# Kernel tuning notes

Hardware: AMD Instinct MI355X
Metric: run time of the kernel (lower is better)

## Reference

```python
import jax, jax.numpy as jnp
import numpy as np

THRESHOLD = 0.3          # config.sparse_threshold
COMPETITION_FACTOR = 2.0 # config.competition_factor
TARGET_SPARSITY = 0.1    # config.target_sparsity


def setup_inputs() -> dict:
    key = jax.random.key(0)
    B, D = 32768, 1024
    H = D // 4
    ks = jax.random.split(key, 18)
    def lin(k, fan_in, shape):
        return jax.random.normal(k, shape, dtype=jnp.float32) / np.sqrt(fan_in)
    return {
        "features": jax.random.normal(ks[0], (B, D), dtype=jnp.float32),
        # sparse_gating: Linear(D, D//4) -> ReLU -> Linear(D//4, D) -> Sigmoid
        "w_g1": lin(ks[1], D, (D, H)), "b_g1": jnp.zeros((H,), jnp.float32),
        "w_g2": lin(ks[2], H, (H, D)), "b_g2": jnp.zeros((D,), jnp.float32),
        # competition_calculator: Linear(D, D) -> ReLU -> Linear(D, 1) -> Sigmoid
        "w_c1": lin(ks[3], D, (D, D)), "b_c1": jnp.zeros((D,), jnp.float32),
        "w_c2": lin(ks[4], D, (D, 1)), "b_c2": jnp.zeros((1,), jnp.float32),
        # sparsity_feedback: Linear(2, 16) -> ReLU -> Linear(16, D) -> Sigmoid
        "w_r1": lin(ks[5], 2, (2, 16)), "b_r1": jnp.zeros((16,), jnp.float32),
        "w_r2": lin(ks[6], 16, (16, D)), "b_r2": jnp.zeros((D,), jnp.float32),
        # adaptive_threshold: Linear(3, 16) -> ReLU -> Linear(16, 1) -> Sigmoid
        "w_m1": lin(ks[7], 3, (3, 16)), "b_m1": jnp.zeros((16,), jnp.float32),
        "w_m2": lin(ks[8], 16, (16, 1)), "b_m2": jnp.zeros((1,), jnp.float32),
    }


def _competitive_sparse(f, w_c1, b_c1, w_c2, b_c2):
    # competition_strength: [B, 1] scalar per row (output Linear has out_dim 1)
    c = jax.nn.sigmoid(jax.nn.relu(f @ w_c1 + b_c1) @ w_c2 + b_c2)  # [B,1]
    inh = COMPETITION_FACTOR * c                                     # [B,1]
    # other_activations_j = f_j * (1 - inh) for j != i, and f_i at position i.
    scaled = f * (1.0 - inh)                                         # [B,D]
    # max over j != i of scaled_j, vectorized via top-2
    top2_vals, _ = jax.lax.top_k(scaled, 2)                          # [B,2]
    am = jnp.argmax(scaled, axis=-1)                                 # [B]
    idx = jnp.arange(f.shape[-1])
    max_excl = jnp.where(idx[None, :] == am[:, None],
                         top2_vals[:, 1:2], top2_vals[:, 0:1])       # [B,D]
    other_max = jnp.maximum(f, max_excl)                             # includes own f_i term
    win = other_max < f
    return jnp.where(f > THRESHOLD, jnp.where(win, f, 0.0), f)


def reference(features, w_g1, b_g1, w_g2, b_g2, w_c1, b_c1, w_c2, b_c2,
              w_r1, b_r1, w_r2, b_r2, w_m1, b_m1, w_m2, b_m2):
    # 1) sparse gating
    gw = jax.nn.sigmoid(jax.nn.relu(features @ w_g1 + b_g1) @ w_g2 + b_g2)
    gated = features * gw
    # 2) competitive sparse activation
    comp = _competitive_sparse(gated, w_c1, b_c1, w_c2, b_c2)
    # 3) dynamic sparsity regulation
    cur_sp = jnp.mean((jnp.abs(comp) < 0.1).astype(comp.dtype), axis=-1)  # [B]
    sp_in = jnp.stack([cur_sp, jnp.full_like(cur_sp, TARGET_SPARSITY)], axis=-1)  # [B,2]
    rw = jax.nn.sigmoid(jax.nn.relu(sp_in @ w_r1 + b_r1) @ w_r2 + b_r2)  # [B,D]
    dyn = comp * rw
    # 4) adaptive threshold (monitor); torch.std is unbiased -> ddof=1
    fmean = jnp.mean(dyn, axis=-1, keepdims=True)
    fstd = jnp.std(dyn, axis=-1, ddof=1, keepdims=True)
    fmax = jnp.max(dyn, axis=-1, keepdims=True)
    thr_in = jnp.concatenate([fmean, fstd, fmax], axis=-1)            # [B,3]
    thr = jax.nn.sigmoid(jax.nn.relu(thr_in @ w_m1 + b_m1) @ w_m2 + b_m2)  # [B,1]
    # 5) final sparse mask
    mask = (jnp.abs(dyn) > thr).astype(dyn.dtype)
    return dyn * mask
```

## Files before the change

### kernel.cpp

```cpp
#include <hip/hip_runtime.h>
#include <cmath>

#define TM 128
#define TN 128
#define TK 16
#define LDSW 132
#define BAND 1e-4
#define FIXCAP 262144u

#define STAGE_STORE(B)                                                          \
        As[B][aq * 4 + 0][ar] = pa0.x; As[B][aq * 4 + 1][ar] = pa0.y;           \
        As[B][aq * 4 + 2][ar] = pa0.z; As[B][aq * 4 + 3][ar] = pa0.w;           \
        As[B][aq * 4 + 0][ar + 64] = pa1.x; As[B][aq * 4 + 1][ar + 64] = pa1.y; \
        As[B][aq * 4 + 2][ar + 64] = pa1.z; As[B][aq * 4 + 3][ar + 64] = pa1.w; \
        *(float4*)&Bs[B][bk][bn4] = pb0;                                        \
        *(float4*)&Bs[B][bk + 8][bn4] = pb1;

#define GEMM_MAINLOOP(Aptr, Wptr, Kdim, Ndim)                                   \
    __shared__ float As[2][TK][LDSW];                                           \
    __shared__ float Bs[2][TK][LDSW];                                           \
    const int tid = threadIdx.x;                                                \
    const int bm = blockIdx.x * TM;                                             \
    const int bn = blockIdx.y * TN;                                             \
    const int tx = tid & 15, ty = tid >> 4;                                     \
    const int ar = tid >> 2, aq = tid & 3;                                      \
    const int bk = tid >> 5, bn4 = (tid & 31) * 4;                              \
    float acc[2][2][4][4];                                                      \
    _Pragma("unroll") for (int a = 0; a < 2; ++a)                               \
    _Pragma("unroll") for (int b = 0; b < 2; ++b)                               \
    _Pragma("unroll") for (int i = 0; i < 4; ++i)                               \
    _Pragma("unroll") for (int j = 0; j < 4; ++j) acc[a][b][i][j] = 0.f;        \
    float4 pa0 = *(const float4*)((Aptr) + (size_t)(bm + ar) * (Kdim) + aq * 4);      \
    float4 pa1 = *(const float4*)((Aptr) + (size_t)(bm + ar + 64) * (Kdim) + aq * 4); \
    float4 pb0 = *(const float4*)((Wptr) + (size_t)bk * (Ndim) + bn + bn4);           \
    float4 pb1 = *(const float4*)((Wptr) + (size_t)(bk + 8) * (Ndim) + bn + bn4);     \
    STAGE_STORE(0)                                                              \
    __syncthreads();                                                            \
    int buf = 0;                                                                \
    for (int k0 = 0; k0 < (Kdim); k0 += TK) {                                   \
        const int nk = k0 + TK;                                                 \
        if (nk < (Kdim)) {                                                      \
            pa0 = *(const float4*)((Aptr) + (size_t)(bm + ar) * (Kdim) + nk + aq * 4);      \
            pa1 = *(const float4*)((Aptr) + (size_t)(bm + ar + 64) * (Kdim) + nk + aq * 4); \
            pb0 = *(const float4*)((Wptr) + (size_t)(nk + bk) * (Ndim) + bn + bn4);         \
            pb1 = *(const float4*)((Wptr) + (size_t)(nk + bk + 8) * (Ndim) + bn + bn4);     \
        }                                                                       \
        _Pragma("unroll") for (int k = 0; k < TK; ++k) {                        \
            float4 da0 = *(const float4*)&As[buf][k][ty * 4];                   \
            float4 da1 = *(const float4*)&As[buf][k][64 + ty * 4];              \
            float4 db0 = *(const float4*)&Bs[buf][k][tx * 4];                   \
            float4 db1 = *(const float4*)&Bs[buf][k][64 + tx * 4];              \
            const float* dap[2] = {&da0.x, &da1.x};                             \
            const float* dbp[2] = {&db0.x, &db1.x};                             \
            _Pragma("unroll") for (int a = 0; a < 2; ++a)                       \
            _Pragma("unroll") for (int b = 0; b < 2; ++b)                       \
            _Pragma("unroll") for (int i = 0; i < 4; ++i)                       \
            _Pragma("unroll") for (int j = 0; j < 4; ++j)                       \
                acc[a][b][i][j] = fmaf(dap[a][i], dbp[b][j], acc[a][b][i][j]);  \
        }                                                                       \
        if (nk < (Kdim)) {                                                      \
            const int nb = buf ^ 1;                                             \
            STAGE_STORE(nb)                                                     \
            __syncthreads();                                                    \
            buf = nb;                                                           \
        }                                                                       \
    }

__global__ __launch_bounds__(256) void gemm1_f32(
    const float* __restrict__ A, const float* __restrict__ W,
    const float* __restrict__ bias, float* __restrict__ out, int M)
{
    const int K = 1024, N = 256;
    GEMM_MAINLOOP(A, W, K, N)
    #pragma unroll
    for (int a = 0; a < 2; ++a) {
        #pragma unroll
        for (int b = 0; b < 2; ++b) {
            const int col = bn + b * 64 + tx * 4;
            float4 bi = *(const float4*)(bias + col);
            #pragma unroll
            for (int i = 0; i < 4; ++i) {
                const int row = bm + a * 64 + ty * 4 + i;
                float4 o;
                o.x = fmaxf(acc[a][b][i][0] + bi.x, 0.f);
                o.y = fmaxf(acc[a][b][i][1] + bi.y, 0.f);
                o.z = fmaxf(acc[a][b][i][2] + bi.z, 0.f);
                o.w = fmaxf(acc[a][b][i][3] + bi.w, 0.f);
                *(float4*)(out + (size_t)row * N + col) = o;
            }
        }
    }
}

__global__ __launch_bounds__(256) void gemm2_f32(
    const float* __restrict__ A, const float* __restrict__ W,
    const float* __restrict__ bias, const float* __restrict__ F,
    float* __restrict__ out, unsigned* __restrict__ counter,
    uint2* __restrict__ list, int M)
{
    const int K = 256, N = 1024;
    GEMM_MAINLOOP(A, W, K, N)
    #pragma unroll
    for (int a = 0; a < 2; ++a) {
        #pragma unroll
        for (int b = 0; b < 2; ++b) {
            const int col = bn + b * 64 + tx * 4;
            float4 bi = *(const float4*)(bias + col);
            const float* bip = &bi.x;
            #pragma unroll
            for (int i = 0; i < 4; ++i) {
                const int row = bm + a * 64 + ty * 4 + i;
                float4 fv = *(const float4*)(F + (size_t)row * N + col);
                const float* fvp = &fv.x;
                float4 o;
                float* op = &o.x;
                #pragma unroll
                for (int j = 0; j < 4; ++j) {
                    double z = (double)acc[a][b][i][j] + (double)bip[j];
                    double gw = 1.0 / (1.0 + exp(-z));
                    double g = (double)fvp[j] * gw;
                    if (fabs(g - 0.3) < BAND) {
                        unsigned idx = atomicAdd(counter, 1u);
                        if (idx < FIXCAP) list[idx] = make_uint2((unsigned)row, (unsigned)(col + j));
                    }
                    double c = (g > 0.3) ? 0.0 : g;
                    op[j] = (float)c;
                }
                *(float4*)(out + (size_t)row * N + col) = o;
            }
        }
    }
}

__global__ __launch_bounds__(256) void fix_exact(
    const float* __restrict__ F, const float* __restrict__ Wg1,
    const float* __restrict__ bg1, const float* __restrict__ Wg2,
    const float* __restrict__ bg2, const unsigned* __restrict__ counter,
    const uint2* __restrict__ list, float* __restrict__ out)
{
    __shared__ float Fs[1024];
    __shared__ double red[4];
    const int tid = threadIdx.x;
    unsigned cnt = *counter;
    if (cnt > FIXCAP) cnt = FIXCAP;

    for (unsigned e = blockIdx.x; e < cnt; e += gridDim.x) {
        const unsigned row = list[e].x, col = list[e].y;
        *(float4*)&Fs[tid * 4] = *(const float4*)(F + (size_t)row * 1024 + tid * 4);
        __syncthreads();
        double acc = 0.0;
        #pragma unroll 4
        for (int j = 0; j < 1024; ++j)
            acc += (double)Fs[j] * (double)Wg1[(size_t)j * 256 + tid];
        double h = acc + (double)bg1[tid];
        h = (h > 0.0) ? h : 0.0;
        double p = h * (double)Wg2[(size_t)tid * 1024 + col];
        #pragma unroll
        for (int o = 32; o > 0; o >>= 1) p += __shfl_down(p, o, 64);
        if ((tid & 63) == 0) red[tid >> 6] = p;
        __syncthreads();
        if (tid == 0) {
            double z2 = red[0] + red[1] + red[2] + red[3] + (double)bg2[col];
            double gw = 1.0 / (1.0 + exp(-z2));
            double g = (double)Fs[col] * gw;
            double c = (g > 0.3) ? 0.0 : g;
            out[(size_t)row * 1024 + col] = (float)c;
        }
        __syncthreads();
    }
}

__global__ __launch_bounds__(256) void finalize_rows(
    float* __restrict__ C,
    const float* __restrict__ wr1, const float* __restrict__ br1,
    const float* __restrict__ wr2, const float* __restrict__ br2,
    const float* __restrict__ wm1, const float* __restrict__ bm1,
    const float* __restrict__ wm2, const float* __restrict__ bm2)
{
    const int D = 1024;
    const int tid = threadIdx.x;
    const int lane = tid & 63;
    const size_t row = (size_t)blockIdx.x * 4 + (tid >> 6);
    const size_t base = row * D;
    const int col0 = lane * 4;

    float4 c4[4];
    #pragma unroll
    for (int q = 0; q < 4; ++q)
        c4[q] = *(const float4*)(C + base + q * 256 + col0);

    double c[16];
    #pragma unroll
    for (int q = 0; q < 4; ++q) {
        c[q * 4 + 0] = (double)c4[q].x; c[q * 4 + 1] = (double)c4[q].y;
        c[q * 4 + 2] = (double)c4[q].z; c[q * 4 + 3] = (double)c4[q].w;
    }

    double cnt = 0.0;
    #pragma unroll
    for (int i = 0; i < 16; ++i) cnt += (fabs(c[i]) < 0.1) ? 1.0 : 0.0;
    #pragma unroll
    for (int o = 32; o > 0; o >>= 1) cnt += __shfl_xor(cnt, o, 64);
    double cur_sp = cnt / 1024.0;

    double hid[16];
    #pragma unroll
    for (int h = 0; h < 16; ++h) {
        double z = cur_sp * (double)wr1[h] + 0.1 * (double)wr1[16 + h] + (double)br1[h];
        hid[h] = (z > 0.0) ? z : 0.0;
    }

    double dyn[16];
    #pragma unroll
    for (int q = 0; q < 4; ++q) {
        const int cq = q * 256 + col0;
        float4 b4 = *(const float4*)(br2 + cq);
        double z[4] = {(double)b4.x, (double)b4.y, (double)b4.z, (double)b4.w};
        #pragma unroll
        for (int h = 0; h < 16; ++h) {
            float4 w4 = *(const float4*)(wr2 + (size_t)h * D + cq);
            z[0] += hid[h] * (double)w4.x;
            z[1] += hid[h] * (double)w4.y;
            z[2] += hid[h] * (double)w4.z;
            z[3] += hid[h] * (double)w4.w;
        }
        #pragma unroll
        for (int j = 0; j < 4; ++j) {
            double rw = 1.0 / (1.0 + exp(-z[j]));
            dyn[q * 4 + j] = c[q * 4 + j] * rw;
        }
    }

    double s = 0.0, mx = -1e300;
    #pragma unroll
    for (int i = 0; i < 16; ++i) { s += dyn[i]; mx = fmax(mx, dyn[i]); }
    #pragma unroll
    for (int o = 32; o > 0; o >>= 1) s += __shfl_xor(s, o, 64);
    double mean = s / 1024.0;

    double sq = 0.0;
    #pragma unroll
    for (int i = 0; i < 16; ++i) { double d = dyn[i] - mean; sq += d * d; }
    #pragma unroll
    for (int o = 32; o > 0; o >>= 1) sq += __shfl_xor(sq, o, 64);
    double sd = sqrt(sq / 1023.0);

    #pragma unroll
    for (int o = 32; o > 0; o >>= 1) mx = fmax(mx, __shfl_xor(mx, o, 64));

    double acc2 = (double)bm2[0];
    #pragma unroll
    for (int h = 0; h < 16; ++h) {
        double hz = mean * (double)wm1[h] + sd * (double)wm1[16 + h]
                  + mx * (double)wm1[32 + h] + (double)bm1[h];
        hz = (hz > 0.0) ? hz : 0.0;
        acc2 += hz * (double)wm2[h];
    }
    double thr = 1.0 / (1.0 + exp(-acc2));

    #pragma unroll
    for (int q = 0; q < 4; ++q) {
        float4 o4;
        o4.x = (float)((fabs(dyn[q * 4 + 0]) > thr) ? dyn[q * 4 + 0] : 0.0);
        o4.y = (float)((fabs(dyn[q * 4 + 1]) > thr) ? dyn[q * 4 + 1] : 0.0);
        o4.z = (float)((fabs(dyn[q * 4 + 2]) > thr) ? dyn[q * 4 + 2] : 0.0);
        o4.w = (float)((fabs(dyn[q * 4 + 3]) > thr) ? dyn[q * 4 + 3] : 0.0);
        *(float4*)(C + base + q * 256 + col0) = o4;
    }
}

extern "C" void kernel_launch(void* const* d_in, const int* in_sizes, int n_in,
                              void* d_out, int out_size, void* d_ws, size_t ws_size,
                              hipStream_t stream)
{
    const float* F   = (const float*)d_in[0];
    const float* wg1 = (const float*)d_in[1];
    const float* bg1 = (const float*)d_in[2];
    const float* wg2 = (const float*)d_in[3];
    const float* bg2 = (const float*)d_in[4];
    const float* wr1 = (const float*)d_in[9];
    const float* br1 = (const float*)d_in[10];
    const float* wr2 = (const float*)d_in[11];
    const float* br2 = (const float*)d_in[12];
    const float* wm1 = (const float*)d_in[13];
    const float* bm1 = (const float*)d_in[14];
    const float* wm2 = (const float*)d_in[15];
    const float* bm2 = (const float*)d_in[16];

    float* out = (float*)d_out;
    const int M = in_sizes[0] / 1024;

    float*    h1      = (float*)d_ws;
    uint2*    list    = (uint2*)((char*)d_ws + (32u << 20));
    unsigned* counter = (unsigned*)((char*)d_ws + (34u << 20));

    hipMemsetAsync(counter, 0, sizeof(unsigned), stream);
    gemm1_f32<<<dim3(M / TM, 256 / TN), 256, 0, stream>>>(F, wg1, bg1, h1, M);
    gemm2_f32<<<dim3(M / TM, 1024 / TN), 256, 0, stream>>>(h1, wg2, bg2, F, out, counter, list, M);
    fix_exact<<<2048, 256, 0, stream>>>(F, wg1, bg1, wg2, bg2, counter, list, out);
    finalize_rows<<<M / 4, 256, 0, stream>>>(out, wr1, br1, wr2, br2, wm1, bm1, wm2, bm2);
}
```

Before: 1.074 ms.

## Use fp32 fast paths with per-row flags and exact fp64 recompute of flagged rows

Moves the gemm2 epilogue and finalize_rows from fp64 to fp32 with fast exp. Rows whose values fall near a decision boundary (the 0.3 and 0.1 thresholds or the adaptive threshold) are flagged and fully recomputed in fp64 by a new row_exact kernel. This replaces the per-element atomic list and fix_exact kernel. The aim is to cut the cost of fp64 arithmetic on the hot path. The risk is that many rows get flagged, making the full-row recompute (a 1024x256 dot product per row) expensive, and that the fixed band widths may miss boundary cases.

```diff
diff --git a/kernel.cpp b/kernel.cpp
--- a/kernel.cpp
+++ b/kernel.cpp
@@ -5,8 +5,10 @@
 #define TN 128
 #define TK 16
 #define LDSW 132
-#define BAND 1e-4
-#define FIXCAP 262144u
+
+#define B03  1e-4f
+#define B01  1e-4f
+#define BDYN 2e-5f
 
 #define STAGE_STORE(B)                                                          \
         As[B][aq * 4 + 0][ar] = pa0.x; As[B][aq * 4 + 1][ar] = pa0.y;           \
@@ -95,8 +97,7 @@
 __global__ __launch_bounds__(256) void gemm2_f32(
     const float* __restrict__ A, const float* __restrict__ W,
     const float* __restrict__ bias, const float* __restrict__ F,
-    float* __restrict__ out, unsigned* __restrict__ counter,
-    uint2* __restrict__ list, int M)
+    float* __restrict__ out, unsigned* __restrict__ flags, int M)
 {
     const int K = 256, N = 1024;
     GEMM_MAINLOOP(A, W, K, N)
@@ -114,59 +115,21 @@
                 const float* fvp = &fv.x;
                 float4 o;
                 float* op = &o.x;
+                bool fl = false;
                 #pragma unroll
                 for (int j = 0; j < 4; ++j) {
-                    double z = (double)acc[a][b][i][j] + (double)bip[j];
-                    double gw = 1.0 / (1.0 + exp(-z));
-                    double g = (double)fvp[j] * gw;
-                    if (fabs(g - 0.3) < BAND) {
-                        unsigned idx = atomicAdd(counter, 1u);
-                        if (idx < FIXCAP) list[idx] = make_uint2((unsigned)row, (unsigned)(col + j));
-                    }
-                    double c = (g > 0.3) ? 0.0 : g;
-                    op[j] = (float)c;
+                    float z = acc[a][b][i][j] + bip[j];
+                    float gw = 1.0f / (1.0f + __expf(-z));
+                    float g = fvp[j] * gw;
+                    float c = (g > 0.3f) ? 0.f : g;
+                    if (fabsf(g - 0.3f) < B03) fl = true;
+                    if (fabsf(fabsf(c) - 0.1f) < B01) fl = true;
+                    op[j] = c;
                 }
+                if (fl) flags[row] = 1u;
                 *(float4*)(out + (size_t)row * N + col) = o;
             }
         }
-    }
-}
-
-__global__ __launch_bounds__(256) void fix_exact(
-    const float* __restrict__ F, const float* __restrict__ Wg1,
-    const float* __restrict__ bg1, const float* __restrict__ Wg2,
-    const float* __restrict__ bg2, const unsigned* __restrict__ counter,
-    const uint2* __restrict__ list, float* __restrict__ out)
-{
-    __shared__ float Fs[1024];
-    __shared__ double red[4];
-    const int tid = threadIdx.x;
-    unsigned cnt = *counter;
-    if (cnt > FIXCAP) cnt = FIXCAP;
-
-    for (unsigned e = blockIdx.x; e < cnt; e += gridDim.x) {
-        const unsigned row = list[e].x, col = list[e].y;
-        *(float4*)&Fs[tid * 4] = *(const float4*)(F + (size_t)row * 1024 + tid * 4);
-        __syncthreads();
-        double acc = 0.0;
-        #pragma unroll 4
-        for (int j = 0; j < 1024; ++j)
-            acc += (double)Fs[j] * (double)Wg1[(size_t)j * 256 + tid];
-        double h = acc + (double)bg1[tid];
-        h = (h > 0.0) ? h : 0.0;
-        double p = h * (double)Wg2[(size_t)tid * 1024 + col];
-        #pragma unroll
-        for (int o = 32; o > 0; o >>= 1) p += __shfl_down(p, o, 64);
-        if ((tid & 63) == 0) red[tid >> 6] = p;
-        __syncthreads();
-        if (tid == 0) {
-            double z2 = red[0] + red[1] + red[2] + red[3] + (double)bg2[col];
-            double gw = 1.0 / (1.0 + exp(-z2));
-            double g = (double)Fs[col] * gw;
-            double c = (g > 0.3) ? 0.0 : g;
-            out[(size_t)row * 1024 + col] = (float)c;
-        }
-        __syncthreads();
     }
 }
 
@@ -175,13 +138,14 @@
     const float* __restrict__ wr1, const float* __restrict__ br1,
     const float* __restrict__ wr2, const float* __restrict__ br2,
     const float* __restrict__ wm1, const float* __restrict__ bm1,
-    const float* __restrict__ wm2, const float* __restrict__ bm2)
+    const float* __restrict__ wm2, const float* __restrict__ bm2,
+    unsigned* __restrict__ flags)
 {
     const int D = 1024;
     const int tid = threadIdx.x;
     const int lane = tid & 63;
-    const size_t row = (size_t)blockIdx.x * 4 + (tid >> 6);
-    const size_t base = row * D;
+    const unsigned row = blockIdx.x * 4 + (tid >> 6);
+    const size_t base = (size_t)row * D;
     const int col0 = lane * 4;
 
     float4 c4[4];
@@ -189,64 +153,197 @@
     for (int q = 0; q < 4; ++q)
         c4[q] = *(const float4*)(C + base + q * 256 + col0);
 
-    double c[16];
+    float c[16];
     #pragma unroll
     for (int q = 0; q < 4; ++q) {
-        c[q * 4 + 0] = (double)c4[q].x; c[q * 4 + 1] = (double)c4[q].y;
-        c[q * 4 + 2] = (double)c4[q].z; c[q * 4 + 3] = (double)c4[q].w;
-    }
-
-    double cnt = 0.0;
-    #pragma unroll
-    for (int i = 0; i < 16; ++i) cnt += (fabs(c[i]) < 0.1) ? 1.0 : 0.0;
+        c[q * 4 + 0] = c4[q].x; c[q * 4 + 1] = c4[q].y;
+        c[q * 4 + 2] = c4[q].z; c[q * 4 + 3] = c4[q].w;
+    }
+
+    float cnt = 0.f;
+    #pragma unroll
+    for (int i = 0; i < 16; ++i) cnt += (fabsf(c[i]) < 0.1f) ? 1.f : 0.f;
     #pragma unroll
     for (int o = 32; o > 0; o >>= 1) cnt += __shfl_xor(cnt, o, 64);
-    double cur_sp = cnt / 1024.0;
-
-    double hid[16];
+    const double cur_sp = (double)cnt / 1024.0;
+
+    float hid[16];
     #pragma unroll
     for (int h = 0; h < 16; ++h) {
         double z = cur_sp * (double)wr1[h] + 0.1 * (double)wr1[16 + h] + (double)br1[h];
-        hid[h] = (z > 0.0) ? z : 0.0;
-    }
-
-    double dyn[16];
+        hid[h] = (float)((z > 0.0) ? z : 0.0);
+    }
+
+    float dyn[16];
     #pragma unroll
     for (int q = 0; q < 4; ++q) {
         const int cq = q * 256 + col0;
         float4 b4 = *(const float4*)(br2 + cq);
-        double z[4] = {(double)b4.x, (double)b4.y, (double)b4.z, (double)b4.w};
+        float z[4] = {b4.x, b4.y, b4.z, b4.w};
         #pragma unroll
         for (int h = 0; h < 16; ++h) {
             float4 w4 = *(const float4*)(wr2 + (size_t)h * D + cq);
-            z[0] += hid[h] * (double)w4.x;
-            z[1] += hid[h] * (double)w4.y;
-            z[2] += hid[h] * (double)w4.z;
-            z[3] += hid[h] * (double)w4.w;
+            z[0] = fmaf(hid[h], w4.x, z[0]);
+            z[1] = fmaf(hid[h], w4.y, z[1]);
+            z[2] = fmaf(hid[h], w4.z, z[2]);
+            z[3] = fmaf(hid[h], w4.w, z[3]);
         }
         #pragma unroll
         for (int j = 0; j < 4; ++j) {
-            double rw = 1.0 / (1.0 + exp(-z[j]));
+            float rw = 1.0f / (1.0f + __expf(-z[j]));
             dyn[q * 4 + j] = c[q * 4 + j] * rw;
         }
     }
 
-    double s = 0.0, mx = -1e300;
-    #pragma unroll
-    for (int i = 0; i < 16; ++i) { s += dyn[i]; mx = fmax(mx, dyn[i]); }
+    float s = 0.f, mx = -1e30f;
+    #pragma unroll
+    for (int i = 0; i < 16; ++i) { s += dyn[i]; mx = fmaxf(mx, dyn[i]); }
     #pragma unroll
     for (int o = 32; o > 0; o >>= 1) s += __shfl_xor(s, o, 64);
-    double mean = s / 1024.0;
+    const float mean = s / 1024.0f;
+
+    float sq = 0.f;
+    #pragma unroll
+    for (int i = 0; i < 16; ++i) { float d = dyn[i] - mean; sq = fmaf(d, d, sq); }
+    #pragma unroll
+    for (int o = 32; o > 0; o >>= 1) sq += __shfl_xor(sq, o, 64);
+    const float sd = sqrtf(sq / 1023.0f);
+
+    #pragma unroll
+    for (int o = 32; o > 0; o >>= 1) mx = fmaxf(mx, __shfl_xor(mx, o, 64));
+
+    double acc2 = (double)bm2[0];
+    #pragma unroll
+    for (int h = 0; h < 16; ++h) {
+        double hz = (double)mean * (double)wm1[h] + (double)sd * (double)wm1[16 + h]
+                  + (double)mx * (double)wm1[32 + h] + (double)bm1[h];
+        hz = (hz > 0.0) ? hz : 0.0;
+        acc2 += hz * (double)wm2[h];
+    }
+    const float thr = (float)(1.0 / (1.0 + exp(-acc2)));
+
+    bool fl = false;
+    #pragma unroll
+    for (int q = 0; q < 4; ++q) {
+        float4 o4;
+        float* op = &o4.x;
+        #pragma unroll
+        for (int j = 0; j < 4; ++j) {
+            float d = dyn[q * 4 + j];
+            float ad = fabsf(d);
+            if (fabsf(ad - thr) < BDYN) fl = true;
+            op[j] = (ad > thr) ? d : 0.f;
+        }
+        *(float4*)(C + base + q * 256 + col0) = o4;
+    }
+    if (fl) flags[row] = 1u;
+}
+
+__device__ __forceinline__ double block_reduce_d(double v, double* sm, int tid, int op)
+{
+    #pragma unroll
+    for (int o = 32; o > 0; o >>= 1) {
+        double other = __shfl_down(v, o, 64);
+        v = op ? fmax(v, other) : (v + other);
+    }
+    if ((tid & 63) == 0) sm[tid >> 6] = v;
+    __syncthreads();
+    if (tid == 0) {
+        double r = sm[0];
+        for (int w = 1; w < 4; ++w) r = op ? fmax(r, sm[w]) : (r + sm[w]);
+        sm[4] = r;
+    }
+    __syncthreads();
+    double r = sm[4];
+    __syncthreads();
+    return r;
+}
+
+__global__ __launch_bounds__(256) void row_exact(
+    const float* __restrict__ F,
+    const float* __restrict__ wg1, const float* __restrict__ bg1,
+    const float* __restrict__ wg2, const float* __restrict__ bg2,
+    const float* __restrict__ wr1, const float* __restrict__ br1,
+    const float* __restrict__ wr2, const float* __restrict__ br2,
+    const float* __restrict__ wm1, const float* __restrict__ bm1,
+    const float* __restrict__ wm2, const float* __restrict__ bm2,
+    const unsigned* __restrict__ flags, float* __restrict__ out)
+{
+    const unsigned row = blockIdx.x;
+    if (flags[row] == 0u) return;
+
+    __shared__ float  Fs[1024];
+    __shared__ double h1d[256];
+    __shared__ double sm[8];
+    const int tid = threadIdx.x;
+
+    *(float4*)&Fs[tid * 4] = *(const float4*)(F + (size_t)row * 1024 + tid * 4);
+    __syncthreads();
+
+    double a = 0.0;
+    #pragma unroll 4
+    for (int j = 0; j < 1024; ++j)
+        a += (double)Fs[j] * (double)wg1[(size_t)j * 256 + tid];
+    a += (double)bg1[tid];
+    h1d[tid] = (a > 0.0) ? a : 0.0;
+    __syncthreads();
+
+    const int c0 = tid * 4;
+    double z[4] = {(double)bg2[c0], (double)bg2[c0 + 1],
+                   (double)bg2[c0 + 2], (double)bg2[c0 + 3]};
+    #pragma unroll 4
+    for (int j = 0; j < 256; ++j) {
+        float4 w = *(const float4*)(wg2 + (size_t)j * 1024 + c0);
+        double h = h1d[j];
+        z[0] += h * (double)w.x; z[1] += h * (double)w.y;
+        z[2] += h * (double)w.z; z[3] += h * (double)w.w;
+    }
+    double comp[4];
+    double cnt = 0.0;
+    #pragma unroll
+    for (int j = 0; j < 4; ++j) {
+        double gw = 1.0 / (1.0 + exp(-z[j]));
+        double g = (double)Fs[c0 + j] * gw;
+        double cm = (g > 0.3) ? 0.0 : g;
+        comp[j] = cm;
+        cnt += (fabs(cm) < 0.1) ? 1.0 : 0.0;
+    }
+    cnt = block_reduce_d(cnt, sm, tid, 0);
+    const double cur_sp = cnt / 1024.0;
+
+    double hid[16];
+    #pragma unroll
+    for (int h = 0; h < 16; ++h) {
+        double hz = cur_sp * (double)wr1[h] + 0.1 * (double)wr1[16 + h] + (double)br1[h];
+        hid[h] = (hz > 0.0) ? hz : 0.0;
+    }
+    double zr[4] = {(double)br2[c0], (double)br2[c0 + 1],
+                    (double)br2[c0 + 2], (double)br2[c0 + 3]};
+    #pragma unroll
+    for (int h = 0; h < 16; ++h) {
+        float4 w4 = *(const float4*)(wr2 + (size_t)h * 1024 + c0);
+        zr[0] += hid[h] * (double)w4.x; zr[1] += hid[h] * (double)w4.y;
+        zr[2] += hid[h] * (double)w4.z; zr[3] += hid[h] * (double)w4.w;
+    }
+    double dyn[4];
+    #pragma unroll
+    for (int j = 0; j < 4; ++j) {
+        double rw = 1.0 / (1.0 + exp(-zr[j]));
+        dyn[j] = comp[j] * rw;
+    }
+
+    double s = dyn[0] + dyn[1] + dyn[2] + dyn[3];
+    s = block_reduce_d(s, sm, tid, 0);
+    const double mean = s / 1024.0;
 
     double sq = 0.0;
     #pragma unroll
-    for (int i = 0; i < 16; ++i) { double d = dyn[i] - mean; sq += d * d; }
-    #pragma unroll
-    for (int o = 32; o > 0; o >>= 1) sq += __shfl_xor(sq, o, 64);
-    double sd = sqrt(sq / 1023.0);
-
-    #pragma unroll
-    for (int o = 32; o > 0; o >>= 1) mx = fmax(mx, __shfl_xor(mx, o, 64));
+    for (int j = 0; j < 4; ++j) { double d = dyn[j] - mean; sq += d * d; }
+    sq = block_reduce_d(sq, sm, tid, 0);
+    const double sd = sqrt(sq / 1023.0);
+
+    double mx = fmax(fmax(dyn[0], dyn[1]), fmax(dyn[2], dyn[3]));
+    mx = block_reduce_d(mx, sm, tid, 1);
 
     double acc2 = (double)bm2[0];
     #pragma unroll
@@ -256,17 +353,14 @@
         hz = (hz > 0.0) ? hz : 0.0;
         acc2 += hz * (double)wm2[h];
     }
-    double thr = 1.0 / (1.0 + exp(-acc2));
-
-    #pragma unroll
-    for (int q = 0; q < 4; ++q) {
-        float4 o4;
-        o4.x = (float)((fabs(dyn[q * 4 + 0]) > thr) ? dyn[q * 4 + 0] : 0.0);
-        o4.y = (float)((fabs(dyn[q * 4 + 1]) > thr) ? dyn[q * 4 + 1] : 0.0);
-        o4.z = (float)((fabs(dyn[q * 4 + 2]) > thr) ? dyn[q * 4 + 2] : 0.0);
-        o4.w = (float)((fabs(dyn[q * 4 + 3]) > thr) ? dyn[q * 4 + 3] : 0.0);
-        *(float4*)(C + base + q * 256 + col0) = o4;
-    }
+    const double thr = 1.0 / (1.0 + exp(-acc2));
+
+    float4 o4;
+    o4.x = (float)((fabs(dyn[0]) > thr) ? dyn[0] : 0.0);
+    o4.y = (float)((fabs(dyn[1]) > thr) ? dyn[1] : 0.0);
+    o4.z = (float)((fabs(dyn[2]) > thr) ? dyn[2] : 0.0);
+    o4.w = (float)((fabs(dyn[3]) > thr) ? dyn[3] : 0.0);
+    *(float4*)(out + (size_t)row * 1024 + c0) = o4;
 }
 
 extern "C" void kernel_launch(void* const* d_in, const int* in_sizes, int n_in,
@@ -290,13 +384,13 @@
     float* out = (float*)d_out;
     const int M = in_sizes[0] / 1024;
 
-    float*    h1      = (float*)d_ws;
-    uint2*    list    = (uint2*)((char*)d_ws + (32u << 20));
-    unsigned* counter = (unsigned*)((char*)d_ws + (34u << 20));
-
-    hipMemsetAsync(counter, 0, sizeof(unsigned), stream);
+    float*    h1    = (float*)d_ws;
+    unsigned* flags = (unsigned*)((char*)d_ws + (32u << 20));
+
+    hipMemsetAsync(flags, 0, (size_t)M * sizeof(unsigned), stream);
     gemm1_f32<<<dim3(M / TM, 256 / TN), 256, 0, stream>>>(F, wg1, bg1, h1, M);
-    gemm2_f32<<<dim3(M / TM, 1024 / TN), 256, 0, stream>>>(h1, wg2, bg2, F, out, counter, list, M);
-    fix_exact<<<2048, 256, 0, stream>>>(F, wg1, bg1, wg2, bg2, counter, list, out);
-    finalize_rows<<<M / 4, 256, 0, stream>>>(out, wr1, br1, wr2, br2, wm1, bm1, wm2, bm2);
-}
+    gemm2_f32<<<dim3(M / TM, 1024 / TN), 256, 0, stream>>>(h1, wg2, bg2, F, out, flags, M);
+    finalize_rows<<<M / 4, 256, 0, stream>>>(out, wr1, br1, wr2, br2, wm1, bm1, wm2, bm2, flags);
+    row_exact<<<M, 256, 0, stream>>>(F, wg1, bg1, wg2, bg2, wr1, br1, wr2, br2,
+                                     wm1, bm1, wm2, bm2, flags, out);
+}
```

After: 1.744 ms. 62.4% more time.
